# Optimization experiments

Measured on AMD Instinct MI355X. Metric: run time of the kernel, lower is better.

The kernel has to match this reference:

```python
import jax, jax.numpy as jnp
import numpy as np

N_VEH, N_PED = 16, 16
DV, DP = 40, 24            # vehicle / pedestrian slot obs dims
N = N_VEH + N_PED          # 32 agents
E, H = 128, 4              # embed_dim, num_heads
DH = E // H                # head_dim = 32
B = 4096
OBS = N_VEH * DV + N_PED * DP + N  # 1056


def setup_inputs() -> dict:
    key = jax.random.key(0)
    ks = jax.random.split(key, 12)
    s = lambda fan_in: 1.0 / np.sqrt(fan_in)
    inp = {
        "global_obs": jax.random.uniform(ks[0], (B, OBS), dtype=jnp.float32),
        # per-type projectors (stored as (in, out) so x @ W + b)
        "Wv": jax.random.uniform(ks[1], (DV, E), jnp.float32, -s(DV), s(DV)),
        "bv": jax.random.uniform(ks[2], (E,), jnp.float32, -s(DV), s(DV)),
        "Wp": jax.random.uniform(ks[3], (DP, E), jnp.float32, -s(DP), s(DP)),
        "bp": jax.random.uniform(ks[4], (E,), jnp.float32, -s(DP), s(DP)),
        # GAT layer 0 / 1: w (E, H*DH), a_src / a_dst (H, DH)
        "w0": jax.random.normal(ks[5], (E, H * DH), jnp.float32) * s(E),
        "asrc0": jax.random.normal(ks[6], (H, DH), jnp.float32) * s(DH),
        "adst0": jax.random.normal(ks[7], (H, DH), jnp.float32) * s(DH),
        "w1": jax.random.normal(ks[8], (E, H * DH), jnp.float32) * s(E),
        "asrc1": jax.random.normal(ks[9], (H, DH), jnp.float32) * s(DH),
        "adst1": jax.random.normal(ks[10], (H, DH), jnp.float32) * s(DH),
    }
    return inp


def _gat(x, alive, w, a_src, a_dst):
    # x: (B,N,E), alive: (B,N) in {0,1}
    b, n, _ = x.shape
    h = (x @ w).reshape(b, n, H, DH)                       # (B,N,H,DH)
    alpha_src = jnp.einsum("bnhd,hd->bnh", h, a_src)       # (B,N,H)
    alpha_dst = jnp.einsum("bnhd,hd->bnh", h, a_dst)
    e = alpha_src[:, :, None, :] + alpha_dst[:, None, :, :]  # (B,Ni,Nj,H)
    e = jnp.where(e > 0, e, 0.2 * e)                       # LeakyReLU(0.2)
    key_mask = alive[:, None, :, None] >= 0.5              # mask over j
    e = jnp.where(key_mask, e, -jnp.inf)
    attn = jax.nn.softmax(e, axis=2)                       # softmax over keys j
    attn = jnp.nan_to_num(attn)
    out = jnp.einsum("bijh,bjhd->bihd", attn, h)           # weighted aggregate
    return out.reshape(b, n, H * DH)                       # concat heads


def reference(global_obs, Wv, bv, Wp, bp, w0, asrc0, adst0, w1, asrc1, adst1):
    b = global_obs.shape[0]
    veh = global_obs[:, : N_VEH * DV].reshape(b, N_VEH, DV)
    ped = global_obs[:, N_VEH * DV : N_VEH * DV + N_PED * DP].reshape(b, N_PED, DP)
    alive_raw = global_obs[:, -N:]
    tokens = jnp.concatenate([veh @ Wv + bv, ped @ Wp + bp], axis=1)  # (B,N,E)
    alive = (alive_raw >= 0.5).astype(jnp.float32)
    all_dead = jnp.sum(alive, axis=1, keepdims=True) < 0.5
    alive = jnp.where(all_dead, jnp.ones_like(alive), alive)
    x = tokens
    for (w, a_s, a_d) in ((w0, asrc0, adst0), (w1, asrc1, adst1)):
        x = jax.nn.elu(_gat(x, alive, w, a_s, a_d))
    aw = alive[:, :, None]
    pooled = jnp.sum(x * aw, axis=1) / jnp.clip(jnp.sum(aw, axis=1), 1.0)
    return pooled
```

## Files before the change

kernel.cpp:

```cpp
#include <hip/hip_runtime.h>


#define NTOK 32
#define EMB  128
#define OBSL 1056
#define XSTR 136
#define HSTR 40
#define TILE 5120

typedef __attribute__((ext_vector_type(8))) short  short8;
typedef __attribute__((ext_vector_type(4))) float  floatx4;
typedef __attribute__((ext_vector_type(2))) unsigned uint2v;

__device__ __forceinline__ short f2bf(float f) {
  union { float f; unsigned u; } v; v.f = f;
  unsigned r = (v.u + 0x7fffu + ((v.u >> 16) & 1u)) >> 16;
  return (short)(unsigned short)r;
}
__device__ __forceinline__ unsigned pk2(float a, float b) {
  unsigned r; asm("v_cvt_pk_bf16_f32 %0, %1, %2" : "=v"(r) : "v"(a), "v"(b)); return r;
}
__device__ __forceinline__ float exp2_hw(float x) {
#if __has_builtin(__builtin_amdgcn_exp2f)
  return __builtin_amdgcn_exp2f(x);
#else
  return exp2f(x);
#endif
}
__device__ __forceinline__ float rcp_hw(float x) {
#if __has_builtin(__builtin_amdgcn_rcpf)
  return __builtin_amdgcn_rcpf(x);
#else
  return 1.0f / x;
#endif
}
__device__ __forceinline__ float elu1(float v) { return v > 0.f ? v : __expf(v) - 1.f; }
__device__ __forceinline__ floatx4 mfma16(short8 a, short8 b, floatx4 c) {
  return __builtin_amdgcn_mfma_f32_16x16x32_bf16(a, b, c, 0, 0, 0);
}

__global__ void prep_weights(const float* __restrict__ Wv, const float* __restrict__ Wp,
                             const float* __restrict__ w0, const float* __restrict__ w1,
                             short* __restrict__ ws) {
  int idx = blockIdx.x * 256 + threadIdx.x;
  if (idx < 8192) {
    int e = idx >> 6, k = idx & 63;
    float v = (k < 40) ? Wv[(size_t)k * EMB + e] : Wp[(size_t)(k - 40) * EMB + e];
    ws[idx] = f2bf(v);
  } else if (idx < 24576) {
    int t = idx - 8192; int e = t >> 7, k = t & 127;
    ws[idx] = f2bf(w0[(size_t)k * EMB + e]);
  } else {
    int t = idx - 24576; int e = t >> 7, k = t & 127;
    ws[idx] = f2bf(w1[(size_t)k * EMB + e]);
  }
}

__global__ __launch_bounds__(256, 6) void gnn_fused(
    const float* __restrict__ obs,
    const float* __restrict__ bv, const float* __restrict__ bp,
    const float* __restrict__ as0, const float* __restrict__ ad0,
    const float* __restrict__ as1, const float* __restrict__ ad1,
    const short* __restrict__ wsb,
    float* __restrict__ out)
{
  __shared__ __align__(16) short s_t[2][TILE];

  const int tid  = threadIdx.x;
  const int lane = tid & 63;
  const int wv   = tid >> 6;
  const int item = wv >> 1;
  const int hw   = wv & 1;
  const int col  = lane & 15;
  const int quad = lane >> 4;
  const int b    = blockIdx.x * 2 + item;

  const float* orow = obs + (size_t)b * OBSL;
  short* xbase = s_t[item];
  short* hbase = &s_t[item][hw * 2560];
  const short8  z8 = {0,0,0,0,0,0,0,0};
  const floatx4 fz = {0.f,0.f,0.f,0.f};

  float flag; float invc;
  {
    float araw = (lane < NTOK) ? orow[1024 + lane] : 0.f;
    bool alv = (lane < NTOK) && (araw >= 0.5f);
    unsigned long long m = __ballot(alv);
    int cnt = __popcll(m);
    flag = alv ? 1.f : 0.f;
    if (cnt == 0) { flag = (lane < NTOK) ? 1.f : 0.f; cnt = NTOK; }
    invc = 1.f / (float)cnt;
  }
  const float alvI0 = __shfl(flag, col);
  const float alvI1 = __shfl(flag, 16 + col);

  #pragma unroll
  for (int it = 0; it < 2; ++it) {
    int c = (hw * 2 + it) * 64 + lane;
    *(short8*)&xbase[(c >> 3) * XSTR + (c & 7) * 8] = z8;
  }
  __syncthreads();
  #pragma unroll
  for (int it = 0; it < 2; ++it) {
    int i4 = (hw * 2 + it) * 64 + lane;
    float4 v = *(const float4*)&orow[i4 * 4];
    int r, k;
    if (i4 < 160) { r = (i4 * 205) >> 11;  k = (i4 - r * 10) * 4; }
    else { int t2 = i4 - 160; int q6 = (t2 * 171) >> 10; r = 16 + q6; k = 40 + (t2 - q6 * 6) * 4; }
    uint2v u; u.x = pk2(v.x, v.y); u.y = pk2(v.z, v.w);
    *(uint2v*)&xbase[r * XSTR + k] = u;
  }
  __syncthreads();

  {
    short8 Bxin[2][2];
    #pragma unroll
    for (int nt = 0; nt < 2; ++nt)
      #pragma unroll
      for (int kt = 0; kt < 2; ++kt)
        Bxin[nt][kt] = *(const short8*)&xbase[(nt * 16 + col) * XSTR + kt * 32 + quad * 8];
    __syncthreads();
    const short* embT = wsb;
    #pragma unroll
    for (int mi = 0; mi < 4; ++mi) {
      const int mtE = hw * 4 + mi;
      short8 A0 = *(const short8*)&embT[(mtE * 16 + col) * 64 + quad * 8];
      short8 A1 = *(const short8*)&embT[(mtE * 16 + col) * 64 + 32 + quad * 8];
      float4 bv4 = *(const float4*)&bv[mtE * 16 + quad * 4];
      float4 bp4 = *(const float4*)&bp[mtE * 16 + quad * 4];
      #pragma unroll
      for (int nt = 0; nt < 2; ++nt) {
        floatx4 acc = fz;
        acc = mfma16(A0, Bxin[nt][0], acc);
        acc = mfma16(A1, Bxin[nt][1], acc);
        float4 bb = nt ? bp4 : bv4;
        uint2v u; u.x = pk2(acc[0] + bb.x, acc[1] + bb.y); u.y = pk2(acc[2] + bb.z, acc[3] + bb.w);
        *(uint2v*)&xbase[(nt * 16 + col) * XSTR + mtE * 16 + quad * 4] = u;
      }
    }
  }

  for (int L = 0; L < 2; ++L) {
    const short* wT  = wsb + 8192 + L * 16384;
    const float* gas = L ? as1 : as0;
    const float* gad = L ? ad1 : ad0;

    __syncthreads();

    floatx4 acc[4][2];
    #pragma unroll
    for (int mi = 0; mi < 4; ++mi) { acc[mi][0] = fz; acc[mi][1] = fz; }
    #pragma unroll
    for (int kt = 0; kt < 4; ++kt) {
      short8 B0 = *(const short8*)&xbase[(col) * XSTR + kt * 32 + quad * 8];
      short8 B1 = *(const short8*)&xbase[(16 + col) * XSTR + kt * 32 + quad * 8];
      #pragma unroll
      for (int mi = 0; mi < 4; ++mi) {
        const int mt = hw * 4 + mi;
        short8 A = *(const short8*)&wT[(mt * 16 + col) * 128 + kt * 32 + quad * 8];
        acc[mi][0] = mfma16(A, B0, acc[mi][0]);
        acc[mi][1] = mfma16(A, B1, acc[mi][1]);
      }
    }

    float psrc[2][2], pdst[2][2];
    #pragma unroll
    for (int hl = 0; hl < 2; ++hl) { psrc[hl][0]=0.f; psrc[hl][1]=0.f; pdst[hl][0]=0.f; pdst[hl][1]=0.f; }
    #pragma unroll
    for (int mi = 0; mi < 4; ++mi) {
      const int mt = hw * 4 + mi;
      const int hl = mi >> 1;
      float4 cs = *(const float4*)&gas[mt * 16 + quad * 4];
      float4 cd = *(const float4*)&gad[mt * 16 + quad * 4];
      #pragma unroll
      for (int nt = 0; nt < 2; ++nt) {
        floatx4 a = acc[mi][nt];
        psrc[hl][nt] += a[0]*cs.x + a[1]*cs.y + a[2]*cs.z + a[3]*cs.w;
        pdst[hl][nt] += a[0]*cd.x + a[1]*cd.y + a[2]*cd.z + a[3]*cd.w;
      }
    }
    __syncthreads();

    #pragma unroll
    for (int mi = 0; mi < 4; ++mi) {
      const int rowloc = mi * 16 + quad * 4;
      #pragma unroll
      for (int nt = 0; nt < 2; ++nt) {
        floatx4 a = acc[mi][nt];
        unsigned u01 = pk2(a[0], a[1]);
        unsigned u23 = pk2(a[2], a[3]);
        unsigned short* hrow = (unsigned short*)&hbase[rowloc * HSTR + nt * 16 + col];
        hrow[0]        = (unsigned short)u01;
        hrow[HSTR]     = (unsigned short)(u01 >> 16);
        hrow[2 * HSTR] = (unsigned short)u23;
        hrow[3 * HSTR] = (unsigned short)(u23 >> 16);
      }
    }

    #pragma unroll
    for (int hl = 0; hl < 2; ++hl)
      #pragma unroll
      for (int nt = 0; nt < 2; ++nt) {
        float vs = psrc[hl][nt]; vs += __shfl_xor(vs, 16); vs += __shfl_xor(vs, 32);
        psrc[hl][nt] = vs * 1.44269504088896340736f;
        float vd = pdst[hl][nt]; vd += __shfl_xor(vd, 16); vd += __shfl_xor(vd, 32);
        pdst[hl][nt] = vd * 1.44269504088896340736f;
      }

    float alv8[8];
    #pragma unroll
    for (int jj = 0; jj < 8; ++jj) alv8[jj] = __shfl(flag, quad * 8 + jj);

    short8 pf[2][2];
    #pragma unroll
    for (int hl = 0; hl < 2; ++hl) {
      float vsel = (quad >> 1) ? pdst[hl][1] : pdst[hl][0];
      float ad8[8];
      #pragma unroll
      for (int jj = 0; jj < 8; ++jj) {
        float v = __shfl(vsel, ((quad >> 1) << 5) + ((quad & 1) << 3) + jj);
        ad8[jj] = (alv8[jj] >= 0.5f) ? v : -1e30f;
      }
      #pragma unroll
      for (int ii = 0; ii < 2; ++ii) {
        float ai = psrc[hl][ii];
        float ev[8]; float sum = 0.f;
        #pragma unroll
        for (int jj = 0; jj < 8; ++jj) {
          float e = ai + ad8[jj];
          e = fmaxf(e, 0.2f * e);
          float p = exp2_hw(e);
          ev[jj] = p; sum += p;
        }
        sum += __shfl_xor(sum, 16);
        sum += __shfl_xor(sum, 32);
        float inv = rcp_hw(sum);
        union { unsigned u4[4]; short8 s; } pu;
        #pragma unroll
        for (int p2 = 0; p2 < 4; ++p2) pu.u4[p2] = pk2(ev[2*p2] * inv, ev[2*p2+1] * inv);
        pf[hl][ii] = pu.s;
      }
    }

    short8 Ah[2][2];
    #pragma unroll
    for (int hl = 0; hl < 2; ++hl)
      #pragma unroll
      for (int mt2 = 0; mt2 < 2; ++mt2)
        Ah[hl][mt2] = *(const short8*)&hbase[(hl * 32 + mt2 * 16 + col) * HSTR + quad * 8];
    if (L == 0) __syncthreads();

    #pragma unroll
    for (int hl = 0; hl < 2; ++hl)
      #pragma unroll
      for (int mt2 = 0; mt2 < 2; ++mt2) {
        floatx4 po[2];
        #pragma unroll
        for (int nt = 0; nt < 2; ++nt) {
          po[nt] = mfma16(Ah[hl][mt2], pf[hl][nt], fz);
        }
        const int ecol = hw * 64 + hl * 32 + mt2 * 16 + quad * 4;
        if (L == 0) {
          #pragma unroll
          for (int nt = 0; nt < 2; ++nt) {
            uint2v u;
            u.x = pk2(elu1(po[nt][0]), elu1(po[nt][1]));
            u.y = pk2(elu1(po[nt][2]), elu1(po[nt][3]));
            *(uint2v*)&xbase[(nt * 16 + col) * XSTR + ecol] = u;
          }
        } else {
          #pragma unroll
          for (int r = 0; r < 4; ++r) {
            float s = elu1(po[0][r]) * alvI0 + elu1(po[1][r]) * alvI1;
            s += __shfl_xor(s, 1); s += __shfl_xor(s, 2);
            s += __shfl_xor(s, 4); s += __shfl_xor(s, 8);
            if (col == 0) out[(size_t)b * EMB + ecol + r] = s * invc;
          }
        }
      }
  }
}

extern "C" void kernel_launch(void* const* d_in, const int* in_sizes, int n_in,
                              void* d_out, int out_size, void* d_ws, size_t ws_size,
                              hipStream_t stream) {
  const float* obs = (const float*)d_in[0];
  const float* Wv  = (const float*)d_in[1];
  const float* bv  = (const float*)d_in[2];
  const float* Wp  = (const float*)d_in[3];
  const float* bp  = (const float*)d_in[4];
  const float* w0  = (const float*)d_in[5];
  const float* as0 = (const float*)d_in[6];
  const float* ad0 = (const float*)d_in[7];
  const float* w1  = (const float*)d_in[8];
  const float* as1 = (const float*)d_in[9];
  const float* ad1 = (const float*)d_in[10];
  float* out = (float*)d_out;
  short* wsb = (short*)d_ws;

  int Bn = in_sizes[0] / OBSL;
  prep_weights<<<160, 256, 0, stream>>>(Wv, Wp, w0, w1, wsb);
  gnn_fused<<<Bn / 2, 256, 0, stream>>>(obs, bv, bp, as0, ad0, as1, ad1, wsb, out);
}
```

Baseline: 143.4 us.

## Process one batch item per block with four waves each owning one head

Changes the work split so each 256-thread block handles a single batch item instead of two, with each of the four waves handling one attention head (32 output columns) rather than two heads. The grid doubles, shared memory per block halves, and per-wave register usage for accumulators and softmax state drops, which could raise occupancy and shorten per-wave critical paths. In exchange each weight fragment is now loaded by more blocks, and block launch and barrier overhead is paid per item.

```diff
diff --git a/kernel.cpp b/kernel.cpp
--- a/kernel.cpp
+++ b/kernel.cpp
@@ -64,20 +64,18 @@
     const short* __restrict__ wsb,
     float* __restrict__ out)
 {
-  __shared__ __align__(16) short s_t[2][TILE];
+  __shared__ __align__(16) short s_t[TILE];
 
   const int tid  = threadIdx.x;
   const int lane = tid & 63;
   const int wv   = tid >> 6;
-  const int item = wv >> 1;
-  const int hw   = wv & 1;
   const int col  = lane & 15;
   const int quad = lane >> 4;
-  const int b    = blockIdx.x * 2 + item;
+  const int b    = blockIdx.x;
 
   const float* orow = obs + (size_t)b * OBSL;
-  short* xbase = s_t[item];
-  short* hbase = &s_t[item][hw * 2560];
+  short* xbase = s_t;
+  short* hbase = &s_t[wv * 1280];
   const short8  z8 = {0,0,0,0,0,0,0,0};
   const floatx4 fz = {0.f,0.f,0.f,0.f};
 
@@ -94,15 +92,13 @@
   const float alvI0 = __shfl(flag, col);
   const float alvI1 = __shfl(flag, 16 + col);
 
-  #pragma unroll
-  for (int it = 0; it < 2; ++it) {
-    int c = (hw * 2 + it) * 64 + lane;
+  {
+    int c = wv * 64 + lane;
     *(short8*)&xbase[(c >> 3) * XSTR + (c & 7) * 8] = z8;
   }
   __syncthreads();
-  #pragma unroll
-  for (int it = 0; it < 2; ++it) {
-    int i4 = (hw * 2 + it) * 64 + lane;
+  {
+    int i4 = wv * 64 + lane;
     float4 v = *(const float4*)&orow[i4 * 4];
     int r, k;
     if (i4 < 160) { r = (i4 * 205) >> 11;  k = (i4 - r * 10) * 4; }
@@ -122,8 +118,8 @@
     __syncthreads();
     const short* embT = wsb;
     #pragma unroll
-    for (int mi = 0; mi < 4; ++mi) {
-      const int mtE = hw * 4 + mi;
+    for (int mi = 0; mi < 2; ++mi) {
+      const int mtE = wv * 2 + mi;
       short8 A0 = *(const short8*)&embT[(mtE * 16 + col) * 64 + quad * 8];
       short8 A1 = *(const short8*)&embT[(mtE * 16 + col) * 64 + 32 + quad * 8];
       float4 bv4 = *(const float4*)&bv[mtE * 16 + quad * 4];
@@ -147,42 +143,40 @@
 
     __syncthreads();
 
-    floatx4 acc[4][2];
-    #pragma unroll
-    for (int mi = 0; mi < 4; ++mi) { acc[mi][0] = fz; acc[mi][1] = fz; }
+    floatx4 acc[2][2];
+    #pragma unroll
+    for (int mi = 0; mi < 2; ++mi) { acc[mi][0] = fz; acc[mi][1] = fz; }
     #pragma unroll
     for (int kt = 0; kt < 4; ++kt) {
       short8 B0 = *(const short8*)&xbase[(col) * XSTR + kt * 32 + quad * 8];
       short8 B1 = *(const short8*)&xbase[(16 + col) * XSTR + kt * 32 + quad * 8];
       #pragma unroll
-      for (int mi = 0; mi < 4; ++mi) {
-        const int mt = hw * 4 + mi;
+      for (int mi = 0; mi < 2; ++mi) {
+        const int mt = wv * 2 + mi;
         short8 A = *(const short8*)&wT[(mt * 16 + col) * 128 + kt * 32 + quad * 8];
         acc[mi][0] = mfma16(A, B0, acc[mi][0]);
         acc[mi][1] = mfma16(A, B1, acc[mi][1]);
       }
     }
 
-    float psrc[2][2], pdst[2][2];
-    #pragma unroll
-    for (int hl = 0; hl < 2; ++hl) { psrc[hl][0]=0.f; psrc[hl][1]=0.f; pdst[hl][0]=0.f; pdst[hl][1]=0.f; }
-    #pragma unroll
-    for (int mi = 0; mi < 4; ++mi) {
-      const int mt = hw * 4 + mi;
-      const int hl = mi >> 1;
+    float psrc[2], pdst[2];
+    psrc[0] = 0.f; psrc[1] = 0.f; pdst[0] = 0.f; pdst[1] = 0.f;
+    #pragma unroll
+    for (int mi = 0; mi < 2; ++mi) {
+      const int mt = wv * 2 + mi;
       float4 cs = *(const float4*)&gas[mt * 16 + quad * 4];
       float4 cd = *(const float4*)&gad[mt * 16 + quad * 4];
       #pragma unroll
       for (int nt = 0; nt < 2; ++nt) {
         floatx4 a = acc[mi][nt];
-        psrc[hl][nt] += a[0]*cs.x + a[1]*cs.y + a[2]*cs.z + a[3]*cs.w;
-        pdst[hl][nt] += a[0]*cd.x + a[1]*cd.y + a[2]*cd.z + a[3]*cd.w;
+        psrc[nt] += a[0]*cs.x + a[1]*cs.y + a[2]*cs.z + a[3]*cs.w;
+        pdst[nt] += a[0]*cd.x + a[1]*cd.y + a[2]*cd.z + a[3]*cd.w;
       }
     }
     __syncthreads();
 
     #pragma unroll
-    for (int mi = 0; mi < 4; ++mi) {
+    for (int mi = 0; mi < 2; ++mi) {
       const int rowloc = mi * 16 + quad * 4;
       #pragma unroll
       for (int nt = 0; nt < 2; ++nt) {
@@ -198,23 +192,20 @@
     }
 
     #pragma unroll
-    for (int hl = 0; hl < 2; ++hl)
-      #pragma unroll
-      for (int nt = 0; nt < 2; ++nt) {
-        float vs = psrc[hl][nt]; vs += __shfl_xor(vs, 16); vs += __shfl_xor(vs, 32);
-        psrc[hl][nt] = vs * 1.44269504088896340736f;
-        float vd = pdst[hl][nt]; vd += __shfl_xor(vd, 16); vd += __shfl_xor(vd, 32);
-        pdst[hl][nt] = vd * 1.44269504088896340736f;
-      }
+    for (int nt = 0; nt < 2; ++nt) {
+      float vs = psrc[nt]; vs += __shfl_xor(vs, 16); vs += __shfl_xor(vs, 32);
+      psrc[nt] = vs * 1.44269504088896340736f;
+      float vd = pdst[nt]; vd += __shfl_xor(vd, 16); vd += __shfl_xor(vd, 32);
+      pdst[nt] = vd * 1.44269504088896340736f;
+    }
 
     float alv8[8];
     #pragma unroll
     for (int jj = 0; jj < 8; ++jj) alv8[jj] = __shfl(flag, quad * 8 + jj);
 
-    short8 pf[2][2];
-    #pragma unroll
-    for (int hl = 0; hl < 2; ++hl) {
-      float vsel = (quad >> 1) ? pdst[hl][1] : pdst[hl][0];
+    short8 pf[2];
+    {
+      float vsel = (quad >> 1) ? pdst[1] : pdst[0];
       float ad8[8];
       #pragma unroll
       for (int jj = 0; jj < 8; ++jj) {
@@ -223,7 +214,7 @@
       }
       #pragma unroll
       for (int ii = 0; ii < 2; ++ii) {
-        float ai = psrc[hl][ii];
+        float ai = psrc[ii];
         float ev[8]; float sum = 0.f;
         #pragma unroll
         for (int jj = 0; jj < 8; ++jj) {
@@ -238,46 +229,42 @@
         union { unsigned u4[4]; short8 s; } pu;
         #pragma unroll
         for (int p2 = 0; p2 < 4; ++p2) pu.u4[p2] = pk2(ev[2*p2] * inv, ev[2*p2+1] * inv);
-        pf[hl][ii] = pu.s;
-      }
-    }
-
-    short8 Ah[2][2];
-    #pragma unroll
-    for (int hl = 0; hl < 2; ++hl)
-      #pragma unroll
-      for (int mt2 = 0; mt2 < 2; ++mt2)
-        Ah[hl][mt2] = *(const short8*)&hbase[(hl * 32 + mt2 * 16 + col) * HSTR + quad * 8];
+        pf[ii] = pu.s;
+      }
+    }
+
+    short8 Ah[2];
+    #pragma unroll
+    for (int mt2 = 0; mt2 < 2; ++mt2)
+      Ah[mt2] = *(const short8*)&hbase[(mt2 * 16 + col) * HSTR + quad * 8];
     if (L == 0) __syncthreads();
 
     #pragma unroll
-    for (int hl = 0; hl < 2; ++hl)
-      #pragma unroll
-      for (int mt2 = 0; mt2 < 2; ++mt2) {
-        floatx4 po[2];
+    for (int mt2 = 0; mt2 < 2; ++mt2) {
+      floatx4 po[2];
+      #pragma unroll
+      for (int nt = 0; nt < 2; ++nt) {
+        po[nt] = mfma16(Ah[mt2], pf[nt], fz);
+      }
+      const int ecol = wv * 32 + mt2 * 16 + quad * 4;
+      if (L == 0) {
         #pragma unroll
         for (int nt = 0; nt < 2; ++nt) {
-          po[nt] = mfma16(Ah[hl][mt2], pf[hl][nt], fz);
+          uint2v u;
+          u.x = pk2(elu1(po[nt][0]), elu1(po[nt][1]));
+          u.y = pk2(elu1(po[nt][2]), elu1(po[nt][3]));
+          *(uint2v*)&xbase[(nt * 16 + col) * XSTR + ecol] = u;
         }
-        const int ecol = hw * 64 + hl * 32 + mt2 * 16 + quad * 4;
-        if (L == 0) {
-          #pragma unroll
-          for (int nt = 0; nt < 2; ++nt) {
-            uint2v u;
-            u.x = pk2(elu1(po[nt][0]), elu1(po[nt][1]));
-            u.y = pk2(elu1(po[nt][2]), elu1(po[nt][3]));
-            *(uint2v*)&xbase[(nt * 16 + col) * XSTR + ecol] = u;
-          }
-        } else {
-          #pragma unroll
-          for (int r = 0; r < 4; ++r) {
-            float s = elu1(po[0][r]) * alvI0 + elu1(po[1][r]) * alvI1;
-            s += __shfl_xor(s, 1); s += __shfl_xor(s, 2);
-            s += __shfl_xor(s, 4); s += __shfl_xor(s, 8);
-            if (col == 0) out[(size_t)b * EMB + ecol + r] = s * invc;
-          }
+      } else {
+        #pragma unroll
+        for (int r = 0; r < 4; ++r) {
+          float s = elu1(po[0][r]) * alvI0 + elu1(po[1][r]) * alvI1;
+          s += __shfl_xor(s, 1); s += __shfl_xor(s, 2);
+          s += __shfl_xor(s, 4); s += __shfl_xor(s, 8);
+          if (col == 0) out[(size_t)b * EMB + ecol + r] = s * invc;
         }
       }
+    }
   }
 }
 
@@ -300,5 +287,5 @@
 
   int Bn = in_sizes[0] / OBSL;
   prep_weights<<<160, 256, 0, stream>>>(Wv, Wp, w0, w1, wsb);
-  gnn_fused<<<Bn / 2, 256, 0, stream>>>(obs, bv, bp, as0, ad0, as1, ad1, wsb, out);
-}
+  gnn_fused<<<Bn, 256, 0, stream>>>(obs, bv, bp, as0, ad0, as1, ad1, wsb, out);
+}
```

New measurement: 130.2 us. 1.1x faster.
